# Kernel tuning notes

Hardware: AMD Instinct MI355X
Metric: run time of the kernel (lower is better)

The kernel has to match this reference:

```python
import jax, jax.numpy as jnp
import numpy as np

# Structure constants C[i, j, k] for the Cl(3,0) geometric product with basis
# order [1, e1, e2, e3, e12, e13, e23, e123]: (a*b)_k = sum_ij a_i b_j C[i,j,k].
_TABLE = [
    (0,0,0,1),(1,1,0,1),(2,2,0,1),(3,3,0,1),(4,4,0,-1),(5,5,0,-1),(6,6,0,-1),(7,7,0,-1),
    (0,1,1,1),(1,0,1,1),(2,4,1,-1),(4,2,1,1),(3,5,1,-1),(5,3,1,1),(6,7,1,-1),(7,6,1,-1),
    (0,2,2,1),(2,0,2,1),(1,4,2,1),(4,1,2,-1),(3,6,2,-1),(6,3,2,1),(5,7,2,1),(7,5,2,1),
    (0,3,3,1),(3,0,3,1),(1,5,3,1),(5,1,3,-1),(2,6,3,1),(6,2,3,-1),(4,7,3,-1),(7,4,3,-1),
    (0,4,4,1),(4,0,4,1),(1,2,4,1),(2,1,4,-1),(3,7,4,1),(7,3,4,1),(5,6,4,-1),(6,5,4,1),
    (0,5,5,1),(5,0,5,1),(1,3,5,1),(3,1,5,-1),(2,7,5,-1),(7,2,5,-1),(4,6,5,1),(6,4,5,-1),
    (0,6,6,1),(6,0,6,1),(2,3,6,1),(3,2,6,-1),(1,7,6,1),(7,1,6,1),(4,5,6,-1),(5,4,6,1),
    (0,7,7,1),(7,0,7,1),(1,6,7,1),(6,1,7,1),(2,5,7,-1),(5,2,7,-1),(3,4,7,1),(4,3,7,1),
]
_C = np.zeros((8, 8, 8), dtype=np.float32)
for _i, _j, _k, _s in _TABLE:
    _C[_i, _j, _k] = _s

B, IN_F, OUT_F = 65536, 64, 64


def setup_inputs() -> dict:
    key = jax.random.key(0)
    ks = jax.random.split(key, 5)
    return {
        "x": jax.random.normal(ks[0], (B, IN_F, 8), dtype=jnp.float32),
        "weight": jax.random.normal(ks[1], (OUT_F, IN_F, 8), dtype=jnp.float32) * 0.02,
        "bias": jnp.zeros((OUT_F, 8), dtype=jnp.float32),
        "row_scale": jax.random.uniform(ks[2], (OUT_F,), dtype=jnp.float32),
        "col_scale": jax.random.uniform(ks[3], (IN_F,), dtype=jnp.float32),
        "bias_shift": jax.random.normal(ks[4], (OUT_F,), dtype=jnp.float32),
    }


def reference(x, weight, bias, row_scale, col_scale, bias_shift):
    C = jnp.asarray(_C)  # [8,8,8] structure constants
    w = weight * row_scale[:, None, None] * col_scale[None, :, None]
    w = jnp.nan_to_num(w, nan=0.0)
    # Fold structure constants into the (small) weight first: wc[o,n,i,k]
    wc = jnp.einsum('onj,ijk->onik', w, C)
    # out[b,o,k] = sum_{n,i} x[b,n,i] * wc[o,n,i,k]  (geometric product + sum over in)
    out = jnp.einsum('bni,onik->bok', x, wc)
    out = out + bias[None]
    out = out.at[..., 0].add(bias_shift[None, :])
    return out
```

## Files before the change

kernel.cpp:

```cpp
#include <hip/hip_runtime.h>
#include <cstdint>

#define M_DIM 65536
#define N_DIM 512
#define K_DIM 512
#define BM 128
#define BN 128
#define BK 32

typedef float f32x4 __attribute__((ext_vector_type(4)));
typedef __bf16 bf16x8 __attribute__((ext_vector_type(8)));
typedef unsigned short us8 __attribute__((ext_vector_type(8)));

__device__ __forceinline__ unsigned short f2bf(float f) {
  unsigned int u = __builtin_bit_cast(unsigned int, f);
  u += 0x7fffu + ((u >> 16) & 1u);
  return (unsigned short)(u >> 16);
}

__device__ __forceinline__ void async_copy16(const void* gptr, void* ldsptr) {
  __builtin_amdgcn_global_load_lds(
      (const __attribute__((address_space(1))) void*)gptr,
      (__attribute__((address_space(3))) void*)ldsptr, 16, 0, 0);
}

__global__ void clifford_prep(const float* __restrict__ weight,
                              const float* __restrict__ bias,
                              const float* __restrict__ row_scale,
                              const float* __restrict__ col_scale,
                              const float* __restrict__ bias_shift,
                              unsigned short* __restrict__ WCT,
                              float* __restrict__ bias2) {
  const int t = blockIdx.x * 256 + threadIdx.x;
  if (t < 512) {
    const int o = t >> 3, k = t & 7;
    bias2[t] = bias[t] + (k == 0 ? bias_shift[o] : 0.0f);
  }
  if (t >= 64 * 64) return;
  const int o = t >> 6, n = t & 63;
  const float rs = row_scale[o], cs = col_scale[n];
  float w[8];
#pragma unroll
  for (int j = 0; j < 8; ++j) {
    float v = weight[(size_t)t * 8 + j] * rs * cs;
    w[j] = (v != v) ? 0.0f : v;
  }
  constexpr int TI[64] = {0,1,2,3,4,5,6,7, 0,1,2,4,3,5,6,7, 0,2,1,4,3,6,5,7,
                          0,3,1,5,2,6,4,7, 0,4,1,2,3,7,5,6, 0,5,1,3,2,7,4,6,
                          0,6,2,3,1,7,4,5, 0,7,1,6,2,5,3,4};
  constexpr int TJ[64] = {0,1,2,3,4,5,6,7, 1,0,4,2,5,3,7,6, 2,0,4,1,6,3,7,5,
                          3,0,5,1,6,2,7,4, 4,0,2,1,7,3,6,5, 5,0,3,1,7,2,6,4,
                          6,0,3,2,7,1,5,4, 7,0,6,1,5,2,4,3};
  constexpr int TK[64] = {0,0,0,0,0,0,0,0, 1,1,1,1,1,1,1,1, 2,2,2,2,2,2,2,2,
                          3,3,3,3,3,3,3,3, 4,4,4,4,4,4,4,4, 5,5,5,5,5,5,5,5,
                          6,6,6,6,6,6,6,6, 7,7,7,7,7,7,7,7};
  constexpr float TS[64] = {1,1,1,1,-1,-1,-1,-1, 1,1,-1,1,-1,1,-1,-1, 1,1,1,-1,-1,1,1,1,
                            1,1,1,-1,1,-1,-1,-1, 1,1,1,-1,1,1,-1,1,  1,1,1,-1,-1,-1,1,-1,
                            1,1,1,-1,1,1,-1,1,   1,1,1,1,-1,-1,1,1};
  float wc[8][8];
#pragma unroll
  for (int i = 0; i < 8; ++i)
#pragma unroll
    for (int k = 0; k < 8; ++k) wc[i][k] = 0.0f;
#pragma unroll
  for (int e = 0; e < 64; ++e) wc[TI[e]][TK[e]] += TS[e] * w[TJ[e]];
#pragma unroll
  for (int k = 0; k < 8; ++k)
#pragma unroll
    for (int i = 0; i < 8; ++i)
      WCT[(size_t)(o * 8 + k) * K_DIM + (n * 8 + i)] = f2bf(wc[i][k]);
}

__global__ __launch_bounds__(256) void clifford_gemm(
    const float* __restrict__ x, const unsigned short* __restrict__ WCT,
    const float* __restrict__ bias2, float* __restrict__ out) {
  __shared__ __align__(16) float As[BM * BK];
  __shared__ __align__(16) unsigned short Bs[BN * BK];

  const int tid = threadIdx.x;
  const int lane = tid & 63;
  const int wv = tid >> 6;

  const int n0 = (blockIdx.x & 3) * BN;
  const size_t m0 = (size_t)(blockIdx.x >> 2) * BM;

  const int a_row = lane >> 3;
  const int a_grp = (lane & 7) ^ a_row;
  const int b_row = lane >> 2;
  const int b_grp = lane & 3;

  const float* xg = x + (m0 + (size_t)wv * 32) * K_DIM;
  float* AsW = &As[(wv * 32) * BK];
  unsigned short* BsW = &Bs[(wv * 32) * BK];

  const int wm = (wv & 1) * 64;
  const int wn = (wv >> 1) * 64;
  const int lm = lane & 15;
  const int kg = lane >> 4;
  const int p0 = (kg << 1) ^ (lm & 7);

  const f32x4 zero = {0.f, 0.f, 0.f, 0.f};
  f32x4 acc[4][4];
#pragma unroll
  for (int i = 0; i < 4; ++i)
#pragma unroll
    for (int j = 0; j < 4; ++j) acc[i][j] = zero;

  for (int ks = 0; ks < K_DIM / BK; ++ks) {
    const int kc = ks * BK;
    __syncthreads();
#pragma unroll
    for (int tslab = 0; tslab < 4; ++tslab) {
      const float* g = xg + (size_t)(tslab * 8 + a_row) * K_DIM + kc + a_grp * 4;
      async_copy16(g, AsW + tslab * 8 * BK);
    }
#pragma unroll
    for (int tslab = 0; tslab < 2; ++tslab) {
      const unsigned short* g =
          WCT + (size_t)(n0 + wv * 32 + tslab * 16 + b_row) * K_DIM + kc + b_grp * 8;
      async_copy16(g, BsW + tslab * 16 * BK);
    }
    __syncthreads();

    bf16x8 af[4], bfr[4];
#pragma unroll
    for (int mi = 0; mi < 4; ++mi) {
      const float* base = &As[(wm + mi * 16 + lm) * BK];
      f32x4 lo = *(const f32x4*)(base + p0 * 4);
      f32x4 hi = *(const f32x4*)(base + (p0 ^ 1) * 4);
      union { bf16x8 v; unsigned short u[8]; } cv;
#pragma unroll
      for (int j = 0; j < 4; ++j) {
        cv.u[j] = f2bf(lo[j]);
        cv.u[4 + j] = f2bf(hi[j]);
      }
      af[mi] = cv.v;
    }
#pragma unroll
    for (int ni = 0; ni < 4; ++ni) {
      us8 raw = *(const us8*)&Bs[(wn + ni * 16 + lm) * BK + kg * 8];
      bfr[ni] = __builtin_bit_cast(bf16x8, raw);
    }
#pragma unroll
    for (int mi = 0; mi < 4; ++mi)
#pragma unroll
      for (int ni = 0; ni < 4; ++ni)
        acc[mi][ni] = __builtin_amdgcn_mfma_f32_16x16x32_bf16(af[mi], bfr[ni],
                                                              acc[mi][ni], 0, 0, 0);
  }

#pragma unroll
  for (int ni = 0; ni < 4; ++ni) {
    const int nn = n0 + wn + ni * 16 + lm;
    const float b2 = bias2[nn];
#pragma unroll
    for (int mi = 0; mi < 4; ++mi) {
#pragma unroll
      for (int r = 0; r < 4; ++r) {
        const size_t mm = m0 + wm + mi * 16 + kg * 4 + r;
        out[mm * N_DIM + nn] = acc[mi][ni][r] + b2;
      }
    }
  }
}

extern "C" void kernel_launch(void* const* d_in, const int* in_sizes, int n_in,
                              void* d_out, int out_size, void* d_ws, size_t ws_size,
                              hipStream_t stream) {
  const float* x          = (const float*)d_in[0];
  const float* weight     = (const float*)d_in[1];
  const float* bias       = (const float*)d_in[2];
  const float* row_scale  = (const float*)d_in[3];
  const float* col_scale  = (const float*)d_in[4];
  const float* bias_shift = (const float*)d_in[5];

  unsigned short* WCT = (unsigned short*)d_ws;
  float* bias2 = (float*)((char*)d_ws + (size_t)N_DIM * K_DIM * 2);

  clifford_prep<<<16, 256, 0, stream>>>(weight, bias, row_scale, col_scale,
                                        bias_shift, WCT, bias2);
  clifford_gemm<<<(M_DIM / BM) * (N_DIM / BN), 256, 0, stream>>>(
      x, WCT, bias2, (float*)d_out);
}
```

Measured before the change: 287.7 us.

## Double-buffer LDS tiles, convert A to bf16 at staging, and remap block order

The GEMM main loop becomes double-buffered. The next B tile is fetched asynchronously into LDS and the next A tile is loaded into registers while the MFMAs on the current tile run, so there is one barrier per step instead of two. A is now converted to bf16 once, when it is written to LDS, rather than after every fragment read. This halves A's LDS footprint and removes conversion work from the compute phase. Block indices are also remapped so that groups of eight M-tiles share N-tiles, which is meant to improve L2 reuse of x. In exchange, A loads now go through registers instead of direct-to-LDS async copies, and the LDS bank swizzle is dropped, which may cause bank conflicts.

```diff
diff --git a/kernel.cpp b/kernel.cpp
--- a/kernel.cpp
+++ b/kernel.cpp
@@ -7,6 +7,7 @@
 #define BM 128
 #define BN 128
 #define BK 32
+#define KSTEPS (K_DIM / BK)
 
 typedef float f32x4 __attribute__((ext_vector_type(4)));
 typedef __bf16 bf16x8 __attribute__((ext_vector_type(8)));
@@ -74,30 +75,31 @@
 __global__ __launch_bounds__(256) void clifford_gemm(
     const float* __restrict__ x, const unsigned short* __restrict__ WCT,
     const float* __restrict__ bias2, float* __restrict__ out) {
-  __shared__ __align__(16) float As[BM * BK];
-  __shared__ __align__(16) unsigned short Bs[BN * BK];
+  __shared__ __align__(16) unsigned short As[2][BM * BK];
+  __shared__ __align__(16) unsigned short Bs[2][BN * BK];
 
   const int tid = threadIdx.x;
   const int lane = tid & 63;
   const int wv = tid >> 6;
 
-  const int n0 = (blockIdx.x & 3) * BN;
-  const size_t m0 = (size_t)(blockIdx.x >> 2) * BM;
-
-  const int a_row = lane >> 3;
-  const int a_grp = (lane & 7) ^ a_row;
+  const int bid = blockIdx.x;
+  const int grp = bid >> 5, r = bid & 31;
+  const size_t m0 = (size_t)(grp * 8 + (r & 7)) * BM;
+  const int n0 = (r >> 3) * BN;
+
+  const int s_row = tid >> 1;
+  const int s_half = tid & 1;
+  const float* ag = x + (m0 + s_row) * (size_t)K_DIM + s_half * 16;
+
   const int b_row = lane >> 2;
   const int b_grp = lane & 3;
-
-  const float* xg = x + (m0 + (size_t)wv * 32) * K_DIM;
-  float* AsW = &As[(wv * 32) * BK];
-  unsigned short* BsW = &Bs[(wv * 32) * BK];
 
   const int wm = (wv & 1) * 64;
   const int wn = (wv >> 1) * 64;
   const int lm = lane & 15;
   const int kg = lane >> 4;
-  const int p0 = (kg << 1) ^ (lm & 7);
+
+  f32x4 ar[4];
 
   const f32x4 zero = {0.f, 0.f, 0.f, 0.f};
   f32x4 acc[4][4];
@@ -106,47 +108,64 @@
 #pragma unroll
     for (int j = 0; j < 4; ++j) acc[i][j] = zero;
 
-  for (int ks = 0; ks < K_DIM / BK; ++ks) {
-    const int kc = ks * BK;
-    __syncthreads();
-#pragma unroll
-    for (int tslab = 0; tslab < 4; ++tslab) {
-      const float* g = xg + (size_t)(tslab * 8 + a_row) * K_DIM + kc + a_grp * 4;
-      async_copy16(g, AsW + tslab * 8 * BK);
-    }
-#pragma unroll
-    for (int tslab = 0; tslab < 2; ++tslab) {
+  auto stageB = [&](int buf, int kc) {
+    unsigned short* dst = &Bs[buf][(wv * 32) * BK];
+#pragma unroll
+    for (int ts = 0; ts < 2; ++ts) {
       const unsigned short* g =
-          WCT + (size_t)(n0 + wv * 32 + tslab * 16 + b_row) * K_DIM + kc + b_grp * 8;
-      async_copy16(g, BsW + tslab * 16 * BK);
-    }
-    __syncthreads();
-
+          WCT + (size_t)(n0 + wv * 32 + ts * 16 + b_row) * K_DIM + kc + b_grp * 8;
+      async_copy16(g, dst + ts * 16 * BK);
+    }
+  };
+  auto loadA = [&](int kc) {
+#pragma unroll
+    for (int j = 0; j < 4; ++j) ar[j] = *(const f32x4*)(ag + kc + j * 4);
+  };
+  auto writeA = [&](int buf) {
+    union { us8 v; unsigned short u[8]; } p0, p1;
+#pragma unroll
+    for (int j = 0; j < 4; ++j) {
+      p0.u[j] = f2bf(ar[0][j]);
+      p0.u[4 + j] = f2bf(ar[1][j]);
+      p1.u[j] = f2bf(ar[2][j]);
+      p1.u[4 + j] = f2bf(ar[3][j]);
+    }
+    unsigned short* dst = &As[buf][s_row * BK + s_half * 16];
+    *(us8*)dst = p0.v;
+    *(us8*)(dst + 8) = p1.v;
+  };
+
+  stageB(0, 0);
+  loadA(0);
+  writeA(0);
+  __syncthreads();
+
+  int buf = 0;
+  for (int ks = 0; ks < KSTEPS; ++ks) {
+    if (ks < KSTEPS - 1) {
+      stageB(buf ^ 1, (ks + 1) * BK);
+      loadA((ks + 1) * BK);
+    }
     bf16x8 af[4], bfr[4];
 #pragma unroll
-    for (int mi = 0; mi < 4; ++mi) {
-      const float* base = &As[(wm + mi * 16 + lm) * BK];
-      f32x4 lo = *(const f32x4*)(base + p0 * 4);
-      f32x4 hi = *(const f32x4*)(base + (p0 ^ 1) * 4);
-      union { bf16x8 v; unsigned short u[8]; } cv;
-#pragma unroll
-      for (int j = 0; j < 4; ++j) {
-        cv.u[j] = f2bf(lo[j]);
-        cv.u[4 + j] = f2bf(hi[j]);
-      }
-      af[mi] = cv.v;
-    }
-#pragma unroll
-    for (int ni = 0; ni < 4; ++ni) {
-      us8 raw = *(const us8*)&Bs[(wn + ni * 16 + lm) * BK + kg * 8];
-      bfr[ni] = __builtin_bit_cast(bf16x8, raw);
-    }
+    for (int mi = 0; mi < 4; ++mi)
+      af[mi] = __builtin_bit_cast(
+          bf16x8, *(const us8*)&As[buf][(wm + mi * 16 + lm) * BK + kg * 8]);
+#pragma unroll
+    for (int ni = 0; ni < 4; ++ni)
+      bfr[ni] = __builtin_bit_cast(
+          bf16x8, *(const us8*)&Bs[buf][(wn + ni * 16 + lm) * BK + kg * 8]);
 #pragma unroll
     for (int mi = 0; mi < 4; ++mi)
 #pragma unroll
       for (int ni = 0; ni < 4; ++ni)
         acc[mi][ni] = __builtin_amdgcn_mfma_f32_16x16x32_bf16(af[mi], bfr[ni],
                                                               acc[mi][ni], 0, 0, 0);
+    if (ks < KSTEPS - 1) {
+      writeA(buf ^ 1);
+      __syncthreads();
+      buf ^= 1;
+    }
   }
 
 #pragma unroll
@@ -156,9 +175,9 @@
 #pragma unroll
     for (int mi = 0; mi < 4; ++mi) {
 #pragma unroll
-      for (int r = 0; r < 4; ++r) {
-        const size_t mm = m0 + wm + mi * 16 + kg * 4 + r;
-        out[mm * N_DIM + nn] = acc[mi][ni][r] + b2;
+      for (int rr = 0; rr < 4; ++rr) {
+        const size_t mm = m0 + wm + mi * 16 + kg * 4 + rr;
+        out[mm * N_DIM + nn] = acc[mi][ni][rr] + b2;
       }
     }
   }
```

Measured after the change: 280.4 us. 1.03x faster.

## Load GEMM operands directly into registers with double-buffered prefetch, swizzle block order

Applied to the files above, without the earlier changes.

Drops the LDS staging and both __syncthreads per K-step. Each wave now loads its A (fp32) and B (bf16) fragments straight from global memory into registers, with a two-stage register double buffer so the next K-slice loads while MFMAs run. Blocks are also remapped into groups of 8 M-tiles by 4 N-tiles to improve L2 reuse of x. The manual bf16 rounding is replaced with the native __bf16 cast. In exchange, A rows are re-fetched by the two waves that share them, global accesses are less coalesced, and register pressure rises.

```diff
diff --git a/kernel.cpp b/kernel.cpp
--- a/kernel.cpp
+++ b/kernel.cpp
@@ -7,6 +7,7 @@
 #define BM 128
 #define BN 128
 #define BK 32
+#define KSTEPS (K_DIM / BK)
 
 typedef float f32x4 __attribute__((ext_vector_type(4)));
 typedef __bf16 bf16x8 __attribute__((ext_vector_type(8)));
@@ -16,12 +17,6 @@
   unsigned int u = __builtin_bit_cast(unsigned int, f);
   u += 0x7fffu + ((u >> 16) & 1u);
   return (unsigned short)(u >> 16);
-}
-
-__device__ __forceinline__ void async_copy16(const void* gptr, void* ldsptr) {
-  __builtin_amdgcn_global_load_lds(
-      (const __attribute__((address_space(1))) void*)gptr,
-      (__attribute__((address_space(3))) void*)ldsptr, 16, 0, 0);
 }
 
 __global__ void clifford_prep(const float* __restrict__ weight,
@@ -74,30 +69,22 @@
 __global__ __launch_bounds__(256) void clifford_gemm(
     const float* __restrict__ x, const unsigned short* __restrict__ WCT,
     const float* __restrict__ bias2, float* __restrict__ out) {
-  __shared__ __align__(16) float As[BM * BK];
-  __shared__ __align__(16) unsigned short Bs[BN * BK];
-
   const int tid = threadIdx.x;
   const int lane = tid & 63;
   const int wv = tid >> 6;
 
-  const int n0 = (blockIdx.x & 3) * BN;
-  const size_t m0 = (size_t)(blockIdx.x >> 2) * BM;
-
-  const int a_row = lane >> 3;
-  const int a_grp = (lane & 7) ^ a_row;
-  const int b_row = lane >> 2;
-  const int b_grp = lane & 3;
-
-  const float* xg = x + (m0 + (size_t)wv * 32) * K_DIM;
-  float* AsW = &As[(wv * 32) * BK];
-  unsigned short* BsW = &Bs[(wv * 32) * BK];
+  const int bid = blockIdx.x;
+  const int grp = bid >> 5, r = bid & 31;
+  const size_t m0 = (size_t)(grp * 8 + (r & 7)) * BM;
+  const int n0 = (r >> 3) * BN;
 
   const int wm = (wv & 1) * 64;
   const int wn = (wv >> 1) * 64;
   const int lm = lane & 15;
   const int kg = lane >> 4;
-  const int p0 = (kg << 1) ^ (lm & 7);
+
+  const float* aBase = x + (m0 + wm + lm) * (size_t)K_DIM + kg * 8;
+  const unsigned short* bBase = WCT + (size_t)(n0 + wn + lm) * K_DIM + kg * 8;
 
   const f32x4 zero = {0.f, 0.f, 0.f, 0.f};
   f32x4 acc[4][4];
@@ -106,48 +93,51 @@
 #pragma unroll
     for (int j = 0; j < 4; ++j) acc[i][j] = zero;
 
-  for (int ks = 0; ks < K_DIM / BK; ++ks) {
-    const int kc = ks * BK;
-    __syncthreads();
+  f32x4 alo[2][4], ahi[2][4];
+  us8 braw[2][4];
+
+#define LOAD_STEP(BUF, KS)                                                   \
+  {                                                                          \
+    _Pragma("unroll") for (int mi = 0; mi < 4; ++mi) {                       \
+      const float* p = aBase + (size_t)mi * 16 * K_DIM + (KS) * BK;          \
+      alo[BUF][mi] = *(const f32x4*)p;                                       \
+      ahi[BUF][mi] = *(const f32x4*)(p + 4);                                 \
+    }                                                                        \
+    _Pragma("unroll") for (int ni = 0; ni < 4; ++ni) {                       \
+      braw[BUF][ni] =                                                        \
+          *(const us8*)(bBase + (size_t)ni * 16 * K_DIM + (KS) * BK);        \
+    }                                                                        \
+  }
+
+#define COMPUTE_STEP(BUF)                                                    \
+  {                                                                          \
+    bf16x8 af[4];                                                            \
+    _Pragma("unroll") for (int mi = 0; mi < 4; ++mi) {                       \
+      union { bf16x8 v; __bf16 e[8]; } cv;                                   \
+      _Pragma("unroll") for (int j = 0; j < 4; ++j) {                        \
+        cv.e[j] = (__bf16)alo[BUF][mi][j];                                   \
+        cv.e[4 + j] = (__bf16)ahi[BUF][mi][j];                               \
+      }                                                                      \
+      af[mi] = cv.v;                                                         \
+    }                                                                        \
+    _Pragma("unroll") for (int mi = 0; mi < 4; ++mi)                         \
+        _Pragma("unroll") for (int ni = 0; ni < 4; ++ni) {                   \
+      acc[mi][ni] = __builtin_amdgcn_mfma_f32_16x16x32_bf16(                 \
+          af[mi], __builtin_bit_cast(bf16x8, braw[BUF][ni]), acc[mi][ni],    \
+          0, 0, 0);                                                          \
+    }                                                                        \
+  }
+
+  LOAD_STEP(0, 0)
 #pragma unroll
-    for (int tslab = 0; tslab < 4; ++tslab) {
-      const float* g = xg + (size_t)(tslab * 8 + a_row) * K_DIM + kc + a_grp * 4;
-      async_copy16(g, AsW + tslab * 8 * BK);
-    }
-#pragma unroll
-    for (int tslab = 0; tslab < 2; ++tslab) {
-      const unsigned short* g =
-          WCT + (size_t)(n0 + wv * 32 + tslab * 16 + b_row) * K_DIM + kc + b_grp * 8;
-      async_copy16(g, BsW + tslab * 16 * BK);
-    }
-    __syncthreads();
-
-    bf16x8 af[4], bfr[4];
-#pragma unroll
-    for (int mi = 0; mi < 4; ++mi) {
-      const float* base = &As[(wm + mi * 16 + lm) * BK];
-      f32x4 lo = *(const f32x4*)(base + p0 * 4);
-      f32x4 hi = *(const f32x4*)(base + (p0 ^ 1) * 4);
-      union { bf16x8 v; unsigned short u[8]; } cv;
-#pragma unroll
-      for (int j = 0; j < 4; ++j) {
-        cv.u[j] = f2bf(lo[j]);
-        cv.u[4 + j] = f2bf(hi[j]);
-      }
-      af[mi] = cv.v;
-    }
-#pragma unroll
-    for (int ni = 0; ni < 4; ++ni) {
-      us8 raw = *(const us8*)&Bs[(wn + ni * 16 + lm) * BK + kg * 8];
-      bfr[ni] = __builtin_bit_cast(bf16x8, raw);
-    }
-#pragma unroll
-    for (int mi = 0; mi < 4; ++mi)
-#pragma unroll
-      for (int ni = 0; ni < 4; ++ni)
-        acc[mi][ni] = __builtin_amdgcn_mfma_f32_16x16x32_bf16(af[mi], bfr[ni],
-                                                              acc[mi][ni], 0, 0, 0);
+  for (int kp = 0; kp < KSTEPS / 2; ++kp) {
+    LOAD_STEP(1, 2 * kp + 1)
+    COMPUTE_STEP(0)
+    if (kp < KSTEPS / 2 - 1) LOAD_STEP(0, 2 * kp + 2)
+    COMPUTE_STEP(1)
   }
+#undef LOAD_STEP
+#undef COMPUTE_STEP
 
 #pragma unroll
   for (int ni = 0; ni < 4; ++ni) {
@@ -156,9 +146,9 @@
 #pragma unroll
     for (int mi = 0; mi < 4; ++mi) {
 #pragma unroll
-      for (int r = 0; r < 4; ++r) {
-        const size_t mm = m0 + wm + mi * 16 + kg * 4 + r;
-        out[mm * N_DIM + nn] = acc[mi][ni][r] + b2;
+      for (int rr = 0; rr < 4; ++rr) {
+        const size_t mm = m0 + wm + mi * 16 + kg * 4 + rr;
+        out[mm * N_DIM + nn] = acc[mi][ni][rr] + b2;
       }
     }
   }
```

After: 390.8 us. 1.36x slower.
